# Optimization experiments

Measured on AMD Instinct MI355X. Metric: run time of the kernel, lower is better.

## Reference

```python
import jax, jax.numpy as jnp
import numpy as np

T = 128
IN_SIZE = 1024
OUT_SIZE = 1024
LMBDA = 0.01          # lmbda_in_in (also used for out_in update, as in source)
MAX_POST = 1.0
MAX_PRE = 1.0
CONN_SPARSITY = 0.1   # in_in_sparsity / out_in_sparsity


def setup_inputs() -> dict:
    key = jax.random.key(0)
    k1, k2, k3, k4, k5 = jax.random.split(key, 5)
    inputs = jax.random.normal(k1, (T, IN_SIZE), dtype=jnp.float32)
    # fixed weights ~ nn.Linear init (uniform +-1/sqrt(fan_in)) * g * sparse mask
    b_in = 1.0 / np.sqrt(IN_SIZE)
    in_in_fixed = jax.random.uniform(k2, (IN_SIZE, IN_SIZE), jnp.float32, -b_in, b_in)
    in_in_fixed = in_in_fixed * (jax.random.uniform(k3, (IN_SIZE, IN_SIZE)) < CONN_SPARSITY).astype(jnp.float32)
    b_out = 1.0 / np.sqrt(IN_SIZE)
    out_in_fixed = jax.random.uniform(k4, (OUT_SIZE, IN_SIZE), jnp.float32, -b_out, b_out)
    out_in_fixed = out_in_fixed * (jax.random.uniform(k5, (OUT_SIZE, IN_SIZE)) < CONN_SPARSITY).astype(jnp.float32)
    return {"inputs": inputs, "in_in_fixed": in_in_fixed, "out_in_fixed": out_in_fixed}


def _renorm(P, max_post, max_pre):
    # row (post) renorm then column (pre) renorm, only where sums exceed cap
    post = P.sum(axis=1)
    P = P * jnp.where(post > max_post, max_post / post, 1.0)[:, None]
    pre = P.sum(axis=0)
    P = P * jnp.where(pre > max_pre, max_pre / pre, 1.0)[None, :]
    return P


def reference(inputs, in_in_fixed, out_in_fixed):
    def step(carry, x):
        in_in_p, out_in_p = carry
        # forward_input path: out = F.linear(in_, out_in)
        out = (out_in_fixed + out_in_p) @ x                      # [OUT_SIZE]
        # Hebbian outer-product updates + renorm homeostasis
        in_in_p = _renorm(in_in_p + LMBDA * jnp.outer(x, x), MAX_POST, MAX_PRE)
        out_in_p = _renorm(out_in_p + LMBDA * jnp.outer(out, x), MAX_POST, MAX_PRE)
        return (in_in_p, out_in_p), out

    init = (jnp.zeros_like(in_in_fixed), jnp.zeros_like(out_in_fixed))
    (in_in_p, out_in_p), outs = jax.lax.scan(step, init, inputs)
    return outs  # [T, OUT_SIZE]
```

## Files before the change

kernel.cpp:

```cpp
#include <hip/hip_runtime.h>


typedef float f32x4 __attribute__((ext_vector_type(4)));
typedef float f32x2 __attribute__((ext_vector_type(2)));
typedef unsigned u32x4 __attribute__((ext_vector_type(4)));

#define T_STEPS 128
#define N 1024
#define GR 16
#define GC 16
#define TB 64
#define NT 256
#define LMBDA 0.01f

__global__ __launch_bounds__(NT) void rf2d_kernel(
    const float* __restrict__ X,
    const float* __restrict__ W,
    float* __restrict__ OUT,
    f32x2* __restrict__ OutP,
    float* __restrict__ Scol,
    unsigned* __restrict__ fAr,
    unsigned* __restrict__ fAc,
    unsigned* __restrict__ fBc,
    unsigned* __restrict__ fBr) {
  __shared__ float Pl[TB * TB];
  __shared__ float f_loc[TB];
  __shared__ float rfl[TB], oll[TB];
  __shared__ float SLc[4][TB];
  __shared__ float SLd[4][TB];
  __shared__ float sxAll[T_STEPS];

  const int tid = threadIdx.x;
  const int b = blockIdx.x;
  const int r = b >> 4, c = b & 15;
  const int grow = r * TB, gcol = c * TB;
  const int r_loc = tid >> 2, q = tid & 3;
  const int c_loc = tid & 63, rg = tid >> 6;

  for (int i = tid; i < TB * TB; i += NT) Pl[i] = 0.f;
  if (tid < TB) f_loc[tid] = 1.f;
  {
    const int rowi = tid >> 1, half = tid & 1;
    const f32x4* Xr = (const f32x4*)(X + (size_t)rowi * N) + half * 128;
    f32x4 acc = {0.f, 0.f, 0.f, 0.f};
    for (int j = 0; j < 128; ++j) acc += Xr[j];
    ((float*)SLc)[tid] = (acc.x + acc.y) + (acc.z + acc.w);
  }
  __syncthreads();
  if (tid < T_STEPS)
    sxAll[tid] = ((float*)SLc)[2 * tid] + ((float*)SLc)[2 * tid + 1];

  f32x4 wr[4];
#pragma unroll
  for (int k = 0; k < 4; ++k)
    wr[k] = *(const f32x4*)(W + (size_t)(grow + r_loc) * N + gcol + 16 * q + 4 * k);

  float wrx = 0.f;
  {
    const f32x4* Xn = (const f32x4*)(X + gcol);
#pragma unroll
    for (int k = 0; k < 4; ++k) {
      f32x4 xv = Xn[4 * q + k];
      wrx += (wr[k].x * xv.x + wr[k].y * xv.y) + (wr[k].z * xv.z + wr[k].w * xv.w);
    }
  }
  __syncthreads();

  for (int t = 0; t < T_STEPS; ++t) {
    const int p = t & 1;
    const unsigned tg = t + 1u;

    float a_out = wrx, a_R = 0.f;
    {
      const f32x4* PlV = (const f32x4*)Pl;
      const f32x4* FV = (const f32x4*)f_loc;
      const f32x4* XV = (const f32x4*)(X + (size_t)t * N + gcol);
#pragma unroll
      for (int k = 0; k < 4; ++k) {
        const int lc = 4 * q + k;
        f32x4 pv = PlV[r_loc * 16 + (lc ^ (r_loc & 15))];
        f32x4 fv = FV[lc];
        f32x4 xv = XV[lc];
        f32x4 pf = pv * fv;
        a_R += (pf.x + pf.y) + (pf.z + pf.w);
        a_out += (pf.x * xv.x + pf.y * xv.y) + (pf.z * xv.z + pf.w * xv.w);
      }
    }
    a_out += __shfl_xor(a_out, 1, 64); a_out += __shfl_xor(a_out, 2, 64);
    a_R   += __shfl_xor(a_R, 1, 64);   a_R   += __shfl_xor(a_R, 2, 64);

    if (q == 0) {
      f32x2 v; v.x = a_out; v.y = a_R;
      f32x2* dst = OutP + (size_t)p * GC * N + (size_t)c * N + grow + r_loc;
      asm volatile("global_store_dwordx2 %0, %1, off sc0 sc1"
                   :: "v"(dst), "v"(v) : "memory");
    }
    __syncthreads();
    if (tid == 0) {
      __hip_atomic_store(&fAr[r * GC + c], tg, __ATOMIC_RELAXED, __HIP_MEMORY_SCOPE_AGENT);
      __hip_atomic_store(&fAc[c * GR + r], tg, __ATOMIC_RELAXED, __HIP_MEMORY_SCOPE_AGENT);
    }

    {
      const unsigned* fp = fAr + r * GC + 4 * q;
      u32x4 fv;
      for (;;) {
        asm volatile("global_load_dwordx4 %0, %1, off sc0 sc1\n\ts_waitcnt vmcnt(0)"
                     : "=v"(fv) : "v"(fp) : "memory");
        __builtin_amdgcn_sched_barrier(0);
        if (fv.x >= tg && fv.y >= tg && fv.z >= tg && fv.w >= tg) break;
        __builtin_amdgcn_s_sleep(1);
      }
    }
    {
      f32x2 v0, v1, v2, v3;
      const f32x2* baseA = OutP + (size_t)p * GC * N + grow + r_loc;
      asm volatile("global_load_dwordx2 %0, %4, off sc0 sc1\n\t"
                   "global_load_dwordx2 %1, %5, off sc0 sc1\n\t"
                   "global_load_dwordx2 %2, %6, off sc0 sc1\n\t"
                   "global_load_dwordx2 %3, %7, off sc0 sc1\n\t"
                   "s_waitcnt vmcnt(0)"
                   : "=v"(v0), "=v"(v1), "=v"(v2), "=v"(v3)
                   : "v"(baseA + (size_t)(4 * q + 0) * N),
                     "v"(baseA + (size_t)(4 * q + 1) * N),
                     "v"(baseA + (size_t)(4 * q + 2) * N),
                     "v"(baseA + (size_t)(4 * q + 3) * N)
                   : "memory");
      __builtin_amdgcn_sched_barrier(0);
      float po = (v0.x + v1.x) + (v2.x + v3.x);
      float pR = (v0.y + v1.y) + (v2.y + v3.y);
      po += __shfl_xor(po, 1, 64); po += __shfl_xor(po, 2, 64);
      pR += __shfl_xor(pR, 1, 64); pR += __shfl_xor(pR, 2, 64);
      float ol = LMBDA * po;
      float R1 = pR + ol * sxAll[t];
      float rf = (R1 > 1.f) ? 1.f / R1 : 1.f;
      if (q == 0) { rfl[r_loc] = rf; oll[r_loc] = ol; }
      if (c == 0 && q == 0) OUT[(size_t)t * N + grow + r_loc] = po;
    }
    if (t == T_STEPS - 1) break;
    __syncthreads();

    {
      const float xc = X[(size_t)t * N + gcol + c_loc];
      const float fc = f_loc[c_loc];
      float cacc = 0.f;
#pragma unroll
      for (int rr = 0; rr < 16; ++rr) {
        const int row = rg * 16 + rr;
        const int idx = row * 64 + ((((c_loc >> 2) ^ (row & 15))) << 2) + (c_loc & 3);
        float v = rfl[row] * (Pl[idx] * fc + oll[row] * xc);
        Pl[idx] = v;
        cacc += v;
      }
      SLc[rg][c_loc] = cacc;
    }
    if (tid < 16) {
      while (__hip_atomic_load(&fAc[c * GR + tid], __ATOMIC_RELAXED,
                               __HIP_MEMORY_SCOPE_AGENT) < tg)
        __builtin_amdgcn_s_sleep(1);
    }
    __syncthreads();

    if (tid < TB) {
      float scol = (SLc[0][tid] + SLc[1][tid]) + (SLc[2][tid] + SLc[3][tid]);
      float* dst = Scol + (size_t)p * GR * N + (size_t)r * N + gcol + tid;
      asm volatile("global_store_dword %0, %1, off sc0 sc1"
                   :: "v"(dst), "v"(scol) : "memory");
    }
    __syncthreads();
    if (tid == 0) {
      __hip_atomic_store(&fBc[c * GR + r], tg, __ATOMIC_RELAXED, __HIP_MEMORY_SCOPE_AGENT);
      __hip_atomic_store(&fBr[r * GC + c], tg, __ATOMIC_RELAXED, __HIP_MEMORY_SCOPE_AGENT);
    }

    wrx = 0.f;
    {
      const f32x4* Xn = (const f32x4*)(X + (size_t)(t + 1) * N + gcol);
#pragma unroll
      for (int k = 0; k < 4; ++k) {
        f32x4 xv = Xn[4 * q + k];
        wrx += (wr[k].x * xv.x + wr[k].y * xv.y) + (wr[k].z * xv.z + wr[k].w * xv.w);
      }
    }

    {
      const unsigned* fp = fBc + c * GR + 4 * rg;
      u32x4 fv;
      for (;;) {
        asm volatile("global_load_dwordx4 %0, %1, off sc0 sc1\n\ts_waitcnt vmcnt(0)"
                     : "=v"(fv) : "v"(fp) : "memory");
        __builtin_amdgcn_sched_barrier(0);
        if (fv.x >= tg && fv.y >= tg && fv.z >= tg && fv.w >= tg) break;
        __builtin_amdgcn_s_sleep(1);
      }
    }
    {
      float u0, u1, u2, u3;
      const float* baseB = Scol + (size_t)p * GR * N + gcol + c_loc;
      asm volatile("global_load_dword %0, %4, off sc0 sc1\n\t"
                   "global_load_dword %1, %5, off sc0 sc1\n\t"
                   "global_load_dword %2, %6, off sc0 sc1\n\t"
                   "global_load_dword %3, %7, off sc0 sc1\n\t"
                   "s_waitcnt vmcnt(0)"
                   : "=v"(u0), "=v"(u1), "=v"(u2), "=v"(u3)
                   : "v"(baseB + (size_t)(4 * rg + 0) * N),
                     "v"(baseB + (size_t)(4 * rg + 1) * N),
                     "v"(baseB + (size_t)(4 * rg + 2) * N),
                     "v"(baseB + (size_t)(4 * rg + 3) * N)
                   : "memory");
      __builtin_amdgcn_sched_barrier(0);
      SLd[rg][c_loc] = (u0 + u1) + (u2 + u3);
    }
    if (tid >= 16 && tid < 32) {
      while (__hip_atomic_load(&fBr[r * GC + (tid - 16)], __ATOMIC_RELAXED,
                               __HIP_MEMORY_SCOPE_AGENT) < tg)
        __builtin_amdgcn_s_sleep(1);
    }
    __syncthreads();
    if (tid < TB) {
      float s = (SLd[0][tid] + SLd[1][tid]) + (SLd[2][tid] + SLd[3][tid]);
      f_loc[tid] = (s > 1.f) ? 1.f / s : 1.f;
    }
    __syncthreads();
  }
}

extern "C" void kernel_launch(void* const* d_in, const int* in_sizes, int n_in,
                              void* d_out, int out_size, void* d_ws, size_t ws_size,
                              hipStream_t stream) {
  const float* X = (const float*)d_in[0];
  const float* W = (const float*)d_in[2];
  float* OUT = (float*)d_out;

  char* ws = (char*)d_ws;
  unsigned* fAr = (unsigned*)ws;
  unsigned* fAc = (unsigned*)(ws + 1024);
  unsigned* fBc = (unsigned*)(ws + 2048);
  unsigned* fBr = (unsigned*)(ws + 3072);
  f32x2* OutP = (f32x2*)(ws + 4096);
  float* Scol = (float*)(ws + 4096 + (size_t)2 * GC * N * sizeof(f32x2));

  hipMemsetAsync(ws, 0, 4096, stream);

  hipLaunchKernelGGL(rf2d_kernel, dim3(GR * GC), dim3(NT), 0, stream,
                     X, W, OUT, OutP, Scol, fAr, fAc, fBc, fBr);
}
```

Baseline: 639.9 us.

## Replace block barriers before flag publication with per-wave flags and cache x in registers

Each wave now publishes its own phase-A flag after waiting for its own stores, instead of a block-wide __syncthreads followed by a single thread storing. Readers poll 64 per-wave flags per row with four vector loads. The phase-B flag is likewise stored by wave 0 right after its Scol store, with no extra barrier. The next step's x slice is kept in registers, which removes a global reload in the matvec. This trades intra-block barriers for wider polling and more flag memory, and aims to cut the cross-block synchronisation latency on each of the 128 serial steps.

```diff
diff --git a/kernel.cpp b/kernel.cpp
--- a/kernel.cpp
+++ b/kernel.cpp
@@ -19,9 +19,9 @@
     float* __restrict__ OUT,
     f32x2* __restrict__ OutP,
     float* __restrict__ Scol,
-    unsigned* __restrict__ fAr,
+    unsigned* __restrict__ fAw,
+    unsigned* __restrict__ fBw,
     unsigned* __restrict__ fAc,
-    unsigned* __restrict__ fBc,
     unsigned* __restrict__ fBr) {
   __shared__ float Pl[TB * TB];
   __shared__ float f_loc[TB];
@@ -36,6 +36,7 @@
   const int grow = r * TB, gcol = c * TB;
   const int r_loc = tid >> 2, q = tid & 3;
   const int c_loc = tid & 63, rg = tid >> 6;
+  const int lane = tid & 63;
 
   for (int i = tid; i < TB * TB; i += NT) Pl[i] = 0.f;
   if (tid < TB) f_loc[tid] = 1.f;
@@ -55,13 +56,15 @@
   for (int k = 0; k < 4; ++k)
     wr[k] = *(const f32x4*)(W + (size_t)(grow + r_loc) * N + gcol + 16 * q + 4 * k);
 
+  f32x4 xn[4];
   float wrx = 0.f;
   {
     const f32x4* Xn = (const f32x4*)(X + gcol);
 #pragma unroll
     for (int k = 0; k < 4; ++k) {
-      f32x4 xv = Xn[4 * q + k];
-      wrx += (wr[k].x * xv.x + wr[k].y * xv.y) + (wr[k].z * xv.z + wr[k].w * xv.w);
+      xn[k] = Xn[4 * q + k];
+      wrx += (wr[k].x * xn[k].x + wr[k].y * xn[k].y) +
+             (wr[k].z * xn[k].z + wr[k].w * xn[k].w);
     }
   }
   __syncthreads();
@@ -74,16 +77,15 @@
     {
       const f32x4* PlV = (const f32x4*)Pl;
       const f32x4* FV = (const f32x4*)f_loc;
-      const f32x4* XV = (const f32x4*)(X + (size_t)t * N + gcol);
 #pragma unroll
       for (int k = 0; k < 4; ++k) {
         const int lc = 4 * q + k;
         f32x4 pv = PlV[r_loc * 16 + (lc ^ (r_loc & 15))];
         f32x4 fv = FV[lc];
-        f32x4 xv = XV[lc];
         f32x4 pf = pv * fv;
         a_R += (pf.x + pf.y) + (pf.z + pf.w);
-        a_out += (pf.x * xv.x + pf.y * xv.y) + (pf.z * xv.z + pf.w * xv.w);
+        a_out += (pf.x * xn[k].x + pf.y * xn[k].y) +
+                 (pf.z * xn[k].z + pf.w * xn[k].w);
       }
     }
     a_out += __shfl_xor(a_out, 1, 64); a_out += __shfl_xor(a_out, 2, 64);
@@ -95,20 +97,30 @@
       asm volatile("global_store_dwordx2 %0, %1, off sc0 sc1"
                    :: "v"(dst), "v"(v) : "memory");
     }
-    __syncthreads();
-    if (tid == 0) {
-      __hip_atomic_store(&fAr[r * GC + c], tg, __ATOMIC_RELAXED, __HIP_MEMORY_SCOPE_AGENT);
-      __hip_atomic_store(&fAc[c * GR + r], tg, __ATOMIC_RELAXED, __HIP_MEMORY_SCOPE_AGENT);
-    }
-
-    {
-      const unsigned* fp = fAr + r * GC + 4 * q;
-      u32x4 fv;
+    asm volatile("s_waitcnt vmcnt(0)" ::: "memory");
+    __builtin_amdgcn_sched_barrier(0);
+    if (lane == 0)
+      __hip_atomic_store(&fAw[r * 64 + c * 4 + rg], tg, __ATOMIC_RELAXED,
+                         __HIP_MEMORY_SCOPE_AGENT);
+
+    {
+      const unsigned* fp = fAw + r * 64 + 16 * q;
+      u32x4 a0, a1, a2, a3;
       for (;;) {
-        asm volatile("global_load_dwordx4 %0, %1, off sc0 sc1\n\ts_waitcnt vmcnt(0)"
-                     : "=v"(fv) : "v"(fp) : "memory");
+        asm volatile("global_load_dwordx4 %0, %4, off sc0 sc1\n\t"
+                     "global_load_dwordx4 %1, %5, off sc0 sc1\n\t"
+                     "global_load_dwordx4 %2, %6, off sc0 sc1\n\t"
+                     "global_load_dwordx4 %3, %7, off sc0 sc1\n\t"
+                     "s_waitcnt vmcnt(0)"
+                     : "=v"(a0), "=v"(a1), "=v"(a2), "=v"(a3)
+                     : "v"(fp), "v"(fp + 4), "v"(fp + 8), "v"(fp + 12)
+                     : "memory");
         __builtin_amdgcn_sched_barrier(0);
-        if (fv.x >= tg && fv.y >= tg && fv.z >= tg && fv.w >= tg) break;
+        bool ok = a0.x >= tg && a0.y >= tg && a0.z >= tg && a0.w >= tg &&
+                  a1.x >= tg && a1.y >= tg && a1.z >= tg && a1.w >= tg &&
+                  a2.x >= tg && a2.y >= tg && a2.z >= tg && a2.w >= tg &&
+                  a3.x >= tg && a3.y >= tg && a3.z >= tg && a3.w >= tg;
+        if (ok) break;
         __builtin_amdgcn_s_sleep(1);
       }
     }
@@ -140,6 +152,10 @@
     if (t == T_STEPS - 1) break;
     __syncthreads();
 
+    if (tid == 0)
+      __hip_atomic_store(&fAc[c * GR + r], tg, __ATOMIC_RELAXED,
+                         __HIP_MEMORY_SCOPE_AGENT);
+
     {
       const float xc = X[(size_t)t * N + gcol + c_loc];
       const float fc = f_loc[c_loc];
@@ -166,25 +182,29 @@
       float* dst = Scol + (size_t)p * GR * N + (size_t)r * N + gcol + tid;
       asm volatile("global_store_dword %0, %1, off sc0 sc1"
                    :: "v"(dst), "v"(scol) : "memory");
-    }
-    __syncthreads();
-    if (tid == 0) {
-      __hip_atomic_store(&fBc[c * GR + r], tg, __ATOMIC_RELAXED, __HIP_MEMORY_SCOPE_AGENT);
-      __hip_atomic_store(&fBr[r * GC + c], tg, __ATOMIC_RELAXED, __HIP_MEMORY_SCOPE_AGENT);
-    }
-
-    wrx = 0.f;
+      asm volatile("s_waitcnt vmcnt(0)" ::: "memory");
+      __builtin_amdgcn_sched_barrier(0);
+      if (lane == 0) {
+        __hip_atomic_store(&fBw[c * GR + r], tg, __ATOMIC_RELAXED,
+                           __HIP_MEMORY_SCOPE_AGENT);
+        __hip_atomic_store(&fBr[r * GC + c], tg, __ATOMIC_RELAXED,
+                           __HIP_MEMORY_SCOPE_AGENT);
+      }
+    }
+
     {
       const f32x4* Xn = (const f32x4*)(X + (size_t)(t + 1) * N + gcol);
+      wrx = 0.f;
 #pragma unroll
       for (int k = 0; k < 4; ++k) {
-        f32x4 xv = Xn[4 * q + k];
-        wrx += (wr[k].x * xv.x + wr[k].y * xv.y) + (wr[k].z * xv.z + wr[k].w * xv.w);
-      }
-    }
-
-    {
-      const unsigned* fp = fBc + c * GR + 4 * rg;
+        xn[k] = Xn[4 * q + k];
+        wrx += (wr[k].x * xn[k].x + wr[k].y * xn[k].y) +
+               (wr[k].z * xn[k].z + wr[k].w * xn[k].w);
+      }
+    }
+
+    {
+      const unsigned* fp = fBw + c * GR + 4 * rg;
       u32x4 fv;
       for (;;) {
         asm volatile("global_load_dwordx4 %0, %1, off sc0 sc1\n\ts_waitcnt vmcnt(0)"
@@ -211,8 +231,8 @@
       __builtin_amdgcn_sched_barrier(0);
       SLd[rg][c_loc] = (u0 + u1) + (u2 + u3);
     }
-    if (tid >= 16 && tid < 32) {
-      while (__hip_atomic_load(&fBr[r * GC + (tid - 16)], __ATOMIC_RELAXED,
+    if (tid >= 64 && tid < 80) {
+      while (__hip_atomic_load(&fBr[r * GC + (tid - 64)], __ATOMIC_RELAXED,
                                __HIP_MEMORY_SCOPE_AGENT) < tg)
         __builtin_amdgcn_s_sleep(1);
     }
@@ -233,15 +253,15 @@
   float* OUT = (float*)d_out;
 
   char* ws = (char*)d_ws;
-  unsigned* fAr = (unsigned*)ws;
-  unsigned* fAc = (unsigned*)(ws + 1024);
-  unsigned* fBc = (unsigned*)(ws + 2048);
-  unsigned* fBr = (unsigned*)(ws + 3072);
-  f32x2* OutP = (f32x2*)(ws + 4096);
-  float* Scol = (float*)(ws + 4096 + (size_t)2 * GC * N * sizeof(f32x2));
-
-  hipMemsetAsync(ws, 0, 4096, stream);
+  unsigned* fAw = (unsigned*)ws;
+  unsigned* fBw = (unsigned*)(ws + 4096);
+  unsigned* fAc = (unsigned*)(ws + 5120);
+  unsigned* fBr = (unsigned*)(ws + 6144);
+  f32x2* OutP = (f32x2*)(ws + 8192);
+  float* Scol = (float*)(ws + 8192 + (size_t)2 * GC * N * sizeof(f32x2));
+
+  hipMemsetAsync(ws, 0, 8192, stream);
 
   hipLaunchKernelGGL(rf2d_kernel, dim3(GR * GC), dim3(NT), 0, stream,
-                     X, W, OUT, OutP, Scol, fAr, fAc, fBc, fBr);
+                     X, W, OUT, OutP, Scol, fAw, fBw, fAc, fBr);
 }
```

Result: slower. 1.106 ms (+72.9%).
